# Kernel optimization log

Measured on AMD Instinct MI355X. Metric: run time of the kernel, lower is better.

Reference implementation:

```python
import jax, jax.numpy as jnp
import numpy as np

DISCOUNT_FACTOR = 0.99
EPS = 1e-8


def setup_inputs() -> dict:
    key = jax.random.key(0)
    k1, k2, k3 = jax.random.split(key, 3)
    B, S = 8192, 1024
    # raw params initialized exactly like the torch module: atanh(target)
    raw_gamma = jnp.arctanh(jnp.array([DISCOUNT_FACTOR], dtype=jnp.float32))
    # create_init_lambda_sequence(0.5, S): linear ramp with mean == AVERAGE_LAMBDA
    lam_init = jnp.linspace(0.1, 0.9, S).astype(jnp.float32)
    raw_lambd = jnp.arctanh(lam_init)
    values = jax.random.normal(k1, (B, S + 1, 1), dtype=jnp.float32)
    rewards = jax.random.normal(k2, (B, S, 1), dtype=jnp.float32)
    dones = jax.random.randint(k3, (B, S, 1), 0, 2).astype(jnp.int32)
    return {
        "raw_gamma": raw_gamma,
        "raw_lambd": raw_lambd,
        "values": values,
        "rewards": rewards,
        "dones": dones,
        "input_seq_len": 1024,
    }


def reference(raw_gamma, raw_lambd, values, rewards, dones, input_seq_len):
    # gamma / lambd properties: tanh then clamp_min(1e-8)
    gamma = jnp.maximum(jnp.tanh(raw_gamma), EPS)[0]            # scalar
    lambd = jnp.maximum(jnp.tanh(raw_lambd), EPS)               # [max_seq_len]
    lam_seq = lambd[-input_seq_len:]                            # [S]

    # ---- update_sum_reward_weights (runs under no_grad in torch) ----
    # backward recurrence: v[t] = gamma * (1 - lam[t] + lam[t] * v[t+1]),  v[S] = 1
    def w_step(v_next, lam_t):
        v_t = gamma * (1.0 - lam_t + lam_t * v_next)
        return v_t, jnp.maximum(1.0 - v_t, EPS)

    _, w = jax.lax.scan(
        w_step,
        jnp.asarray(1.0, values.dtype),
        jax.lax.stop_gradient(lam_seq),
        reverse=True,
    )  # w: [S]
    srw = w / jnp.maximum(w.mean(), EPS)
    sum_reward_weights = jax.lax.stop_gradient(srw)[None, :, None]  # [1, S, 1]

    # ---- calculate_lambda_returns ----
    # ret[t] = r[t] + gamma*(1-done[t]) * ((1-lam[t])*V[t+1] + lam[t]*ret[t+1])
    d = dones.astype(values.dtype)
    v_next = values[:, 1:, :]                                   # [B, S, 1]
    xs = (
        jnp.swapaxes(rewards, 0, 1),   # [S, B, 1]
        jnp.swapaxes(d, 0, 1),         # [S, B, 1]
        jnp.swapaxes(v_next, 0, 1),    # [S, B, 1]
        lam_seq,                       # [S]
    )

    def r_step(ret_next, x):
        r, dn, vn, lam = x
        ret = r + gamma * (1.0 - dn) * ((1.0 - lam) * vn + lam * ret_next)
        return ret, ret

    _, rets = jax.lax.scan(r_step, values[:, -1, :], xs, reverse=True)  # [S, B, 1]
    lambda_returns = jnp.swapaxes(rets, 0, 1)                           # [B, S, 1]
    return lambda_returns, sum_reward_weights
```

## Files before the change

### kernel.cpp

```cpp
#include <hip/hip_runtime.h>
#include <math.h>

#define EPSF 1e-8f

__device__ __forceinline__ void suffix_scan64(float& A, float& B, int lane) {
#pragma unroll
    for (int d = 1; d < 64; d <<= 1) {
        float Ao = __shfl_down(A, d);
        float Bo = __shfl_down(B, d);
        if (lane + d < 64) {
            A = fmaf(B, Ao, A);
            B = B * Bo;
        }
    }
}

__global__ __launch_bounds__(256, 8)
void td_lambda_kernel(const float* __restrict__ raw_gamma,
                      const float* __restrict__ raw_lambd, int lam_off,
                      const float* __restrict__ values,
                      const float* __restrict__ rewards,
                      const int* __restrict__ dones,
                      float* __restrict__ out,
                      int B, int S, int rowBlocks)
{
    const float gamma = fmaxf(tanhf(raw_gamma[0]), EPSF);
    const int lane = threadIdx.x & 63;

    if ((int)blockIdx.x == rowBlocks) {
        if (threadIdx.x >= 64) return;
        const int NC = S / 64;

        float carry = 1.0f;
        float partial = 0.0f;
        for (int c = NC - 1; c >= 0; --c) {
            int t = c * 64 + lane;
            float lam = fmaxf(tanhf(raw_lambd[lam_off + t]), EPSF);
            float A = gamma * (1.0f - lam);
            float Bc = gamma * lam;
            suffix_scan64(A, Bc, lane);
            float v = fmaf(Bc, carry, A);
            partial += fmaxf(1.0f - v, EPSF);
            carry = __shfl(v, 0);
        }
#pragma unroll
        for (int d = 32; d; d >>= 1) partial += __shfl_xor(partial, d);
        float inv = 1.0f / fmaxf(partial / (float)S, EPSF);

        carry = 1.0f;
        size_t base = (size_t)B * (size_t)S;
        for (int c = NC - 1; c >= 0; --c) {
            int t = c * 64 + lane;
            float lam = fmaxf(tanhf(raw_lambd[lam_off + t]), EPSF);
            float A = gamma * (1.0f - lam);
            float Bc = gamma * lam;
            suffix_scan64(A, Bc, lane);
            float v = fmaf(Bc, carry, A);
            out[base + t] = fmaxf(1.0f - v, EPSF) * inv;
            carry = __shfl(v, 0);
        }
        return;
    }

    int b = blockIdx.x * 4 + (threadIdx.x >> 6);
    if (b >= B) return;

    const float* rrow = rewards + (size_t)b * S;
    const int*   drow = dones   + (size_t)b * S;
    const float* vrow = values  + (size_t)b * (S + 1);
    float*       orow = out     + (size_t)b * S;

    float carry = vrow[S];

    for (int t0 = S - 256; t0 >= 0; t0 -= 256) {
        int tb = t0 + lane * 4;
        float4 r4 = *(const float4*)(rrow + tb);
        int4   d4 = *(const int4*)(drow + tb);
        float v1 = vrow[tb + 1];
        float v2 = vrow[tb + 2];
        float v3 = vrow[tb + 3];
        float v4 = vrow[tb + 4];

        float a0, a1, a2, a3, b0, b1, b2, b3;
        {
            float lam, gd;
            gd  = gamma * (1.0f - (float)d4.x);
            lam = fmaxf(tanhf(raw_lambd[lam_off + tb + 0]), EPSF);
            b0 = gd * lam; a0 = fmaf(gd * (1.0f - lam), v1, r4.x);
            gd  = gamma * (1.0f - (float)d4.y);
            lam = fmaxf(tanhf(raw_lambd[lam_off + tb + 1]), EPSF);
            b1 = gd * lam; a1 = fmaf(gd * (1.0f - lam), v2, r4.y);
            gd  = gamma * (1.0f - (float)d4.z);
            lam = fmaxf(tanhf(raw_lambd[lam_off + tb + 2]), EPSF);
            b2 = gd * lam; a2 = fmaf(gd * (1.0f - lam), v3, r4.z);
            gd  = gamma * (1.0f - (float)d4.w);
            lam = fmaxf(tanhf(raw_lambd[lam_off + tb + 3]), EPSF);
            b3 = gd * lam; a3 = fmaf(gd * (1.0f - lam), v4, r4.w);
        }

        float A = a3, Bc = b3;
        A = fmaf(b2, A, a2); Bc *= b2;
        A = fmaf(b1, A, a1); Bc *= b1;
        A = fmaf(b0, A, a0); Bc *= b0;

        suffix_scan64(A, Bc, lane);

        float EA = __shfl_down(A, 1);
        float EB = __shfl_down(Bc, 1);
        if (lane == 63) { EA = 0.0f; EB = 1.0f; }

        float x  = fmaf(EB, carry, EA);
        float o3 = fmaf(b3, x,  a3);
        float o2 = fmaf(b2, o3, a2);
        float o1 = fmaf(b1, o2, a1);
        float o0 = fmaf(b0, o1, a0);
        *(float4*)(orow + tb) = make_float4(o0, o1, o2, o3);

        carry = __shfl(o0, 0);
    }
}

extern "C" void kernel_launch(void* const* d_in, const int* in_sizes, int n_in,
                              void* d_out, int out_size, void* d_ws, size_t ws_size,
                              hipStream_t stream) {
    const float* raw_gamma = (const float*)d_in[0];
    const float* raw_lambd = (const float*)d_in[1];
    const float* values    = (const float*)d_in[2];
    const float* rewards   = (const float*)d_in[3];
    const int*   dones     = (const int*)d_in[4];
    float* out = (float*)d_out;

    int n_v = in_sizes[2];
    int n_r = in_sizes[3];
    int B = n_v - n_r;
    int S = n_r / B;
    int lam_off = in_sizes[1] - S;

    int rowBlocks = (B + 3) / 4;
    dim3 grid(rowBlocks + 1);
    dim3 block(256);
    td_lambda_kernel<<<grid, block, 0, stream>>>(
        raw_gamma, raw_lambd, lam_off, values, rewards, dones,
        out, B, S, rowBlocks);
}
```

Measured before the change: 152.5 us.

## Precompute lambda coefficients in prep kernel and scan full rows in one pass

Moves the tanh-based gamma*lambda coefficient computation and the sum-reward-weights scan into a separate single-block prep kernel that writes coefficients to workspace. The main kernel then gives each lane 16 consecutive timesteps and does one wave-wide scan per row, instead of four sequential 256-element chunks each carrying a value across chunks. This removes per-element tanh and the serial chunk loop, and lets all loads for a row be issued up front. The cost is an extra launch, a dependency on workspace, more registers per thread, and a hardcoded S=1024 layout (16 per lane times 64 lanes).

```diff
diff --git a/kernel.cpp b/kernel.cpp
--- a/kernel.cpp
+++ b/kernel.cpp
@@ -2,6 +2,8 @@
 #include <math.h>
 
 #define EPSF 1e-8f
+
+typedef float fvec4 __attribute__((ext_vector_type(4), aligned(4)));
 
 __device__ __forceinline__ void suffix_scan64(float& A, float& B, int lane) {
 #pragma unroll
@@ -15,109 +17,123 @@
     }
 }
 
-__global__ __launch_bounds__(256, 8)
-void td_lambda_kernel(const float* __restrict__ raw_gamma,
-                      const float* __restrict__ raw_lambd, int lam_off,
-                      const float* __restrict__ values,
-                      const float* __restrict__ rewards,
-                      const int* __restrict__ dones,
-                      float* __restrict__ out,
-                      int B, int S, int rowBlocks)
+__global__ __launch_bounds__(256)
+void prep_kernel(const float* __restrict__ raw_gamma,
+                 const float* __restrict__ raw_lambd, int lam_off,
+                 float* __restrict__ gl, float* __restrict__ gol,
+                 float* __restrict__ srw_out, int S)
 {
+    __shared__ float s_gl[1024];
+    __shared__ float s_gol[1024];
     const float gamma = fmaxf(tanhf(raw_gamma[0]), EPSF);
+    for (int t = threadIdx.x; t < S; t += 256) {
+        float lam = fmaxf(tanhf(raw_lambd[lam_off + t]), EPSF);
+        float g1 = gamma * lam;
+        float g0 = gamma - g1;
+        gl[t] = g1;  gol[t] = g0;
+        s_gl[t] = g1; s_gol[t] = g0;
+    }
+    __syncthreads();
+    if (threadIdx.x >= 64) return;
+    const int lane = threadIdx.x;
+    const int base = lane << 4;
+
+    float a[16], b[16];
+#pragma unroll
+    for (int j = 0; j < 16; ++j) { a[j] = s_gol[base + j]; b[j] = s_gl[base + j]; }
+
+    float A = a[15], Bc = b[15];
+#pragma unroll
+    for (int j = 14; j >= 0; --j) { A = fmaf(b[j], A, a[j]); Bc *= b[j]; }
+    suffix_scan64(A, Bc, lane);
+    float EA = __shfl_down(A, 1);
+    float EB = __shfl_down(Bc, 1);
+    if (lane == 63) { EA = 0.0f; EB = 1.0f; }
+
+    float v = fmaf(EB, 1.0f, EA);
+    float w[16];
+    float sum = 0.0f;
+#pragma unroll
+    for (int j = 15; j >= 0; --j) {
+        v = fmaf(b[j], v, a[j]);
+        w[j] = fmaxf(1.0f - v, EPSF);
+        sum += w[j];
+    }
+#pragma unroll
+    for (int d = 32; d; d >>= 1) sum += __shfl_xor(sum, d);
+    float inv = 1.0f / fmaxf(sum / (float)S, EPSF);
+#pragma unroll
+    for (int j = 0; j < 16; ++j) srw_out[base + j] = w[j] * inv;
+}
+
+__global__ __launch_bounds__(256, 4)
+void td_main(const float* __restrict__ gl, const float* __restrict__ gol,
+             const float* __restrict__ values,
+             const float* __restrict__ rewards,
+             const int* __restrict__ dones,
+             float* __restrict__ out, int B, int S)
+{
     const int lane = threadIdx.x & 63;
-
-    if ((int)blockIdx.x == rowBlocks) {
-        if (threadIdx.x >= 64) return;
-        const int NC = S / 64;
-
-        float carry = 1.0f;
-        float partial = 0.0f;
-        for (int c = NC - 1; c >= 0; --c) {
-            int t = c * 64 + lane;
-            float lam = fmaxf(tanhf(raw_lambd[lam_off + t]), EPSF);
-            float A = gamma * (1.0f - lam);
-            float Bc = gamma * lam;
-            suffix_scan64(A, Bc, lane);
-            float v = fmaf(Bc, carry, A);
-            partial += fmaxf(1.0f - v, EPSF);
-            carry = __shfl(v, 0);
-        }
-#pragma unroll
-        for (int d = 32; d; d >>= 1) partial += __shfl_xor(partial, d);
-        float inv = 1.0f / fmaxf(partial / (float)S, EPSF);
-
-        carry = 1.0f;
-        size_t base = (size_t)B * (size_t)S;
-        for (int c = NC - 1; c >= 0; --c) {
-            int t = c * 64 + lane;
-            float lam = fmaxf(tanhf(raw_lambd[lam_off + t]), EPSF);
-            float A = gamma * (1.0f - lam);
-            float Bc = gamma * lam;
-            suffix_scan64(A, Bc, lane);
-            float v = fmaf(Bc, carry, A);
-            out[base + t] = fmaxf(1.0f - v, EPSF) * inv;
-            carry = __shfl(v, 0);
-        }
-        return;
-    }
-
-    int b = blockIdx.x * 4 + (threadIdx.x >> 6);
+    const int b = blockIdx.x * 4 + (threadIdx.x >> 6);
     if (b >= B) return;
 
     const float* rrow = rewards + (size_t)b * S;
     const int*   drow = dones   + (size_t)b * S;
     const float* vrow = values  + (size_t)b * (S + 1);
     float*       orow = out     + (size_t)b * S;
+    const int base = lane << 4;
 
-    float carry = vrow[S];
+    float4 r4[4]; int4 dd[4]; fvec4 v4[4]; float4 g1[4]; float4 g0[4];
+#pragma unroll
+    for (int k = 0; k < 4; ++k) {
+        r4[k] = *(const float4*)(rrow + base + 4 * k);
+        dd[k] = *(const int4*)(drow + base + 4 * k);
+        v4[k] = *(const fvec4*)(vrow + base + 4 * k);
+        g1[k] = *(const float4*)(gl + base + 4 * k);
+        g0[k] = *(const float4*)(gol + base + 4 * k);
+    }
+    float vS = vrow[S];
+    float vb = __shfl_down(v4[0].x, 1);
+    if (lane == 63) vb = vS;
 
-    for (int t0 = S - 256; t0 >= 0; t0 -= 256) {
-        int tb = t0 + lane * 4;
-        float4 r4 = *(const float4*)(rrow + tb);
-        int4   d4 = *(const int4*)(drow + tb);
-        float v1 = vrow[tb + 1];
-        float v2 = vrow[tb + 2];
-        float v3 = vrow[tb + 3];
-        float v4 = vrow[tb + 4];
+    float a[16], bb[16];
+#pragma unroll
+    for (int k = 0; k < 4; ++k) {
+        float vn0 = v4[k].y, vn1 = v4[k].z, vn2 = v4[k].w;
+        float vn3 = (k < 3) ? v4[k + 1].x : vb;
+        float vn[4] = {vn0, vn1, vn2, vn3};
+        float rr[4] = {r4[k].x, r4[k].y, r4[k].z, r4[k].w};
+        int   di[4] = {dd[k].x, dd[k].y, dd[k].z, dd[k].w};
+        float G1[4] = {g1[k].x, g1[k].y, g1[k].z, g1[k].w};
+        float G0[4] = {g0[k].x, g0[k].y, g0[k].z, g0[k].w};
+#pragma unroll
+        for (int j = 0; j < 4; ++j) {
+            float nd = 1.0f - (float)di[j];
+            bb[4 * k + j] = G1[j] * nd;
+            a[4 * k + j]  = fmaf(G0[j] * vn[j], nd, rr[j]);
+        }
+    }
 
-        float a0, a1, a2, a3, b0, b1, b2, b3;
-        {
-            float lam, gd;
-            gd  = gamma * (1.0f - (float)d4.x);
-            lam = fmaxf(tanhf(raw_lambd[lam_off + tb + 0]), EPSF);
-            b0 = gd * lam; a0 = fmaf(gd * (1.0f - lam), v1, r4.x);
-            gd  = gamma * (1.0f - (float)d4.y);
-            lam = fmaxf(tanhf(raw_lambd[lam_off + tb + 1]), EPSF);
-            b1 = gd * lam; a1 = fmaf(gd * (1.0f - lam), v2, r4.y);
-            gd  = gamma * (1.0f - (float)d4.z);
-            lam = fmaxf(tanhf(raw_lambd[lam_off + tb + 2]), EPSF);
-            b2 = gd * lam; a2 = fmaf(gd * (1.0f - lam), v3, r4.z);
-            gd  = gamma * (1.0f - (float)d4.w);
-            lam = fmaxf(tanhf(raw_lambd[lam_off + tb + 3]), EPSF);
-            b3 = gd * lam; a3 = fmaf(gd * (1.0f - lam), v4, r4.w);
-        }
+    float A = a[15], Bc = bb[15];
+#pragma unroll
+    for (int j = 14; j >= 0; --j) { A = fmaf(bb[j], A, a[j]); Bc *= bb[j]; }
 
-        float A = a3, Bc = b3;
-        A = fmaf(b2, A, a2); Bc *= b2;
-        A = fmaf(b1, A, a1); Bc *= b1;
-        A = fmaf(b0, A, a0); Bc *= b0;
+    suffix_scan64(A, Bc, lane);
+    float EA = __shfl_down(A, 1);
+    float EB = __shfl_down(Bc, 1);
+    if (lane == 63) { EA = 0.0f; EB = 1.0f; }
+    float x = fmaf(EB, vS, EA);
 
-        suffix_scan64(A, Bc, lane);
-
-        float EA = __shfl_down(A, 1);
-        float EB = __shfl_down(Bc, 1);
-        if (lane == 63) { EA = 0.0f; EB = 1.0f; }
-
-        float x  = fmaf(EB, carry, EA);
-        float o3 = fmaf(b3, x,  a3);
-        float o2 = fmaf(b2, o3, a2);
-        float o1 = fmaf(b1, o2, a1);
-        float o0 = fmaf(b0, o1, a0);
-        *(float4*)(orow + tb) = make_float4(o0, o1, o2, o3);
-
-        carry = __shfl(o0, 0);
+    float o[16];
+#pragma unroll
+    for (int j = 15; j >= 0; --j) {
+        x = fmaf(bb[j], x, a[j]);
+        o[j] = x;
     }
+#pragma unroll
+    for (int k = 0; k < 4; ++k)
+        *(float4*)(orow + base + 4 * k) =
+            make_float4(o[4 * k], o[4 * k + 1], o[4 * k + 2], o[4 * k + 3]);
 }
 
 extern "C" void kernel_launch(void* const* d_in, const int* in_sizes, int n_in,
@@ -136,10 +152,12 @@
     int S = n_r / B;
     int lam_off = in_sizes[1] - S;
 
-    int rowBlocks = (B + 3) / 4;
-    dim3 grid(rowBlocks + 1);
-    dim3 block(256);
-    td_lambda_kernel<<<grid, block, 0, stream>>>(
-        raw_gamma, raw_lambd, lam_off, values, rewards, dones,
-        out, B, S, rowBlocks);
+    float* gl  = (float*)d_ws;
+    float* gol = gl + S;
+    float* srw_out = out + (size_t)B * S;
+
+    prep_kernel<<<1, 256, 0, stream>>>(raw_gamma, raw_lambd, lam_off,
+                                       gl, gol, srw_out, S);
+    td_main<<<(B + 3) / 4, 256, 0, stream>>>(gl, gol, values, rewards, dones,
+                                             out, B, S);
 }
```

Result: no change. 152.2 us (-0.2%).
